# Kernel optimization log

Measured on AMD Instinct MI355X. Metric: run time of the kernel, lower is better.

Reference implementation:

```python
import jax, jax.numpy as jnp
import numpy as np

TEMP = 0.05
DIAG_PENALTY = 1e12
EPS = 1e-8  # matches torch F.cosine_similarity eps


def setup_inputs() -> dict:
    key = jax.random.key(0)
    x = jax.random.normal(key, (8192, 768), dtype=jnp.float32)
    return {"x": x}


def reference(x):
    n = x.shape[0]
    # labels: swap adjacent pairs -> i - (i%2)*2 + 1  (i.e. i XOR 1)
    idx = jnp.arange(n)
    labels = idx - (idx % 2) * 2 + 1
    # cosine similarity matrix via normalize + GEMM (same math as broadcasted
    # F.cosine_similarity: dot(x_i, x_j) / (max(||x_i||,eps) * max(||x_j||,eps)))
    norms = jnp.maximum(jnp.linalg.norm(x, axis=-1, keepdims=True), EPS)
    xn = x / norms
    sim = xn @ xn.T                                   # [N, N]
    sim = sim - jnp.eye(n, dtype=sim.dtype) * DIAG_PENALTY
    logits = sim / TEMP
    # mean cross-entropy with stable log-softmax
    logp = jax.nn.log_softmax(logits, axis=-1)
    loss = -jnp.mean(jnp.take_along_axis(logp, labels[:, None], axis=-1))
    return loss
```

## Files before the change

### kernel.cpp

```cpp
#include <hip/hip_runtime.h>
#include <hip/hip_bf16.h>

#define N 8192
#define D 768
#define TEMP_INV 20.0f
#define NTILES 2080

typedef __attribute__((ext_vector_type(4))) float f32x4;
typedef __attribute__((ext_vector_type(4))) int i32x4;
typedef __attribute__((ext_vector_type(8))) int i32x8;

#define SCALE1 0x7F7F7F7F


__global__ __launch_bounds__(256) void norm_kernel(
    const float* __restrict__ x, unsigned char* __restrict__ xn,
    float* __restrict__ rowsum) {
  int t = threadIdx.x, w = t >> 6, lane = t & 63;
  int row = blockIdx.x * 4 + w;
  const float4* xr = (const float4*)(x + (size_t)row * D);
  float4 v[3];
  v[0] = xr[lane];
  v[1] = xr[lane + 64];
  v[2] = xr[lane + 128];
  float ss = 0.0f;
#pragma unroll
  for (int i = 0; i < 3; ++i)
    ss += v[i].x * v[i].x + v[i].y * v[i].y + v[i].z * v[i].z + v[i].w * v[i].w;
#pragma unroll
  for (int m = 32; m; m >>= 1) ss += __shfl_xor(ss, m);
  float inv = 1.0f / fmaxf(sqrtf(ss), 1e-8f);
  unsigned int* xo = (unsigned int*)(xn + (size_t)row * D);
#pragma unroll
  for (int i = 0; i < 3; ++i) {
    int p = __builtin_amdgcn_cvt_pk_fp8_f32(v[i].x * inv, v[i].y * inv, 0, false);
    p = __builtin_amdgcn_cvt_pk_fp8_f32(v[i].z * inv, v[i].w * inv, p, true);
    xo[lane + 64 * i] = p;
  }
  if (t < 4) rowsum[blockIdx.x * 4 + t] = 0.0f;
}

__global__ __launch_bounds__(256, 4) void sim_kernel(
    const unsigned char* __restrict__ xn, float* __restrict__ rowsum,
    float* __restrict__ pos) {
  static const short stbase[37] = {
      0, 36, 100, 164, 228, 292, 356, 420,
      484, 520, 584, 648, 712, 776, 840,
      904, 940, 1004, 1068, 1132, 1196,
      1260, 1296, 1360, 1424, 1488,
      1552, 1588, 1652, 1716,
      1780, 1816, 1880,
      1944, 1980,
      2044, 2080};
  static const char sti[36] = {0,0,0,0,0,0,0,0, 1,1,1,1,1,1,1, 2,2,2,2,2,2,
                               3,3,3,3,3, 4,4,4,4, 5,5,5, 6,6, 7};
  static const char stj[36] = {0,1,2,3,4,5,6,7, 1,2,3,4,5,6,7, 2,3,4,5,6,7,
                               3,4,5,6,7, 4,5,6,7, 5,6,7, 6,7, 7};
  int b = blockIdx.x;
  int p = 260 * (b & 7) + (b >> 3);
  int s = 0;
  while ((int)stbase[s + 1] <= p) ++s;
  int wofs = p - stbase[s];
  int SI = sti[s], SJ = stj[s];
  int bi, bj;
  if (SI == SJ) {
    int di = 0, cum = 0;
    while (wofs >= cum + (8 - di)) { cum += 8 - di; ++di; }
    bi = SI * 8 + di;
    bj = SI * 8 + di + (wofs - cum);
  } else {
    bi = SI * 8 + (wofs >> 3);
    bj = SJ * 8 + (wofs & 7);
  }

  __shared__ i32x4 As4[128 * 8];
  __shared__ i32x4 Bs4[128 * 8];

  int t = threadIdx.x;
  int w = t >> 6, lane = t & 63;
  int q = lane >> 4, cl = lane & 15;
  int wm = w >> 1, wn = w & 1;

  f32x4 acc[4][4] = {};

  int ulog = (((t & 7) ^ ((t >> 3) & 7))) * 16;
  const unsigned char* Ab = xn + (size_t)(bi * 128 + (t >> 3)) * D + ulog;
  const unsigned char* Bb = xn + (size_t)(bj * 128 + (t >> 3)) * D + ulog;

  int u0 = (2 * q) ^ (cl & 7);
  int u1 = u0 ^ 1;

  for (int kc = 0; kc < 6; ++kc) {
    int k0 = kc * 128;
#pragma unroll
    for (int rr = 0; rr < 4; ++rr) {
      __builtin_amdgcn_global_load_lds(
          (const __attribute__((address_space(1))) unsigned int*)(Ab + (size_t)(rr * 32) * D + k0),
          (__attribute__((address_space(3))) unsigned int*)(As4 + rr * 256 + t), 16, 0, 0);
      __builtin_amdgcn_global_load_lds(
          (const __attribute__((address_space(1))) unsigned int*)(Bb + (size_t)(rr * 32) * D + k0),
          (__attribute__((address_space(3))) unsigned int*)(Bs4 + rr * 256 + t), 16, 0, 0);
    }
    __syncthreads();

    union Frag { i32x8 v8; struct { i32x4 lo, hi; } pr; };
    Frag a[4], bb[4];
#pragma unroll
    for (int m = 0; m < 4; ++m) {
      int rowb = (wm * 64 + m * 16 + cl) * 8;
      a[m].pr.lo = As4[rowb + u0];
      a[m].pr.hi = As4[rowb + u1];
    }
#pragma unroll
    for (int n = 0; n < 4; ++n) {
      int rowb = (wn * 64 + n * 16 + cl) * 8;
      bb[n].pr.lo = Bs4[rowb + u0];
      bb[n].pr.hi = Bs4[rowb + u1];
    }
#pragma unroll
    for (int m = 0; m < 4; ++m)
#pragma unroll
      for (int n = 0; n < 4; ++n)
        acc[m][n] = __builtin_amdgcn_mfma_scale_f32_16x16x128_f8f6f4(
            a[m].v8, bb[n].v8, acc[m][n], 0, 0, 0, SCALE1, 0, SCALE1);
    __syncthreads();
  }

  int gi0 = bi * 128 + wm * 64;
  int gj0 = bj * 128 + wn * 64;

  float rowp[4][4] = {};
  float colp[4] = {};

  if (bi == bj) {
#pragma unroll
    for (int m = 0; m < 4; ++m)
#pragma unroll
      for (int n = 0; n < 4; ++n)
#pragma unroll
        for (int r = 0; r < 4; ++r) {
          float sv = acc[m][n][r];
          int row = gi0 + m * 16 + q * 4 + r;
          int col = gj0 + n * 16 + cl;
          float e = __expf(TEMP_INV * sv - 20.0f);
          if (col == row) e = 0.0f;
          if (col == (row ^ 1)) pos[row] = TEMP_INV * sv;
          rowp[m][r] += e;
        }
  } else {
#pragma unroll
    for (int m = 0; m < 4; ++m)
#pragma unroll
      for (int n = 0; n < 4; ++n)
#pragma unroll
        for (int r = 0; r < 4; ++r) {
          float e = __expf(TEMP_INV * acc[m][n][r] - 20.0f);
          rowp[m][r] += e;
          colp[n] += e;
        }
  }

#pragma unroll
  for (int m = 0; m < 4; ++m)
#pragma unroll
    for (int r = 0; r < 4; ++r) {
      float v = rowp[m][r];
      v += __shfl_xor(v, 1);
      v += __shfl_xor(v, 2);
      v += __shfl_xor(v, 4);
      v += __shfl_xor(v, 8);
      if (cl == 0) atomicAdd(&rowsum[gi0 + m * 16 + q * 4 + r], v);
    }
  if (bi != bj) {
#pragma unroll
    for (int n = 0; n < 4; ++n) {
      float v = colp[n];
      v += __shfl_xor(v, 16);
      v += __shfl_xor(v, 32);
      if (q == 0) atomicAdd(&rowsum[gj0 + n * 16 + cl], v);
    }
  }
}

__global__ __launch_bounds__(1024) void loss_kernel(
    const float* __restrict__ rowsum, const float* __restrict__ pos,
    float* __restrict__ out) {
  int t = threadIdx.x;
  const float4* r4 = (const float4*)rowsum;
  const float4* p4 = (const float4*)pos;
  float acc = 0.0f;
#pragma unroll
  for (int it = 0; it < 2; ++it) {
    int i = t + it * 1024;
    float4 r = r4[i], pp = p4[i];
    acc += 80.0f + __logf(r.x) + __logf(r.y) + __logf(r.z) + __logf(r.w)
           - pp.x - pp.y - pp.z - pp.w;
  }
#pragma unroll
  for (int m = 32; m; m >>= 1) acc += __shfl_xor(acc, m);
  __shared__ float wsum[16];
  if ((t & 63) == 0) wsum[t >> 6] = acc;
  __syncthreads();
  if (t == 0) {
    float tot = 0.0f;
#pragma unroll
    for (int i = 0; i < 16; ++i) tot += wsum[i];
    out[0] = tot / (float)N;
  }
}

extern "C" void kernel_launch(void* const* d_in, const int* in_sizes, int n_in,
                              void* d_out, int out_size, void* d_ws, size_t ws_size,
                              hipStream_t stream) {
  const float* x = (const float*)d_in[0];
  float* rowsum = (float*)d_ws;
  float* pos = rowsum + N;
  unsigned char* xn = (unsigned char*)(rowsum + 2 * N + 16);

  norm_kernel<<<N / 4, 256, 0, stream>>>(x, xn, rowsum);
  sim_kernel<<<NTILES, 256, 0, stream>>>(xn, rowsum, pos);
  loss_kernel<<<1, 1024, 0, stream>>>(rowsum, pos, (float*)d_out);
}
```

Before: 125.0 us.

## Load MFMA fragments directly from global memory, dropping LDS staging and barriers

The similarity kernel no longer stages A and B tiles in shared memory through global_load_lds with barriers. Each lane now loads its FP8 MFMA fragments straight from global memory, the k-loop is fully unrolled, and the launch bound is relaxed to 2 blocks per CU so the compiler has more registers. This removes the LDS round trip and the __syncthreads stalls. In exchange, the tiles shared by the four waves are fetched redundantly from L2/global with less coalesced 32-byte accesses, and occupancy drops.

After: 193.1 us. +54.5%, slower.

```diff
diff --git a/kernel.cpp b/kernel.cpp
--- a/kernel.cpp
+++ b/kernel.cpp
@@ -40,7 +40,7 @@
   if (t < 4) rowsum[blockIdx.x * 4 + t] = 0.0f;
 }
 
-__global__ __launch_bounds__(256, 4) void sim_kernel(
+__global__ __launch_bounds__(256, 2) void sim_kernel(
     const unsigned char* __restrict__ xn, float* __restrict__ rowsum,
     float* __restrict__ pos) {
   static const short stbase[37] = {
@@ -73,9 +73,6 @@
     bj = SJ * 8 + (wofs & 7);
   }
 
-  __shared__ i32x4 As4[128 * 8];
-  __shared__ i32x4 Bs4[128 * 8];
-
   int t = threadIdx.x;
   int w = t >> 6, lane = t & 63;
   int q = lane >> 4, cl = lane & 15;
@@ -83,39 +80,25 @@
 
   f32x4 acc[4][4] = {};
 
-  int ulog = (((t & 7) ^ ((t >> 3) & 7))) * 16;
-  const unsigned char* Ab = xn + (size_t)(bi * 128 + (t >> 3)) * D + ulog;
-  const unsigned char* Bb = xn + (size_t)(bj * 128 + (t >> 3)) * D + ulog;
-
-  int u0 = (2 * q) ^ (cl & 7);
-  int u1 = u0 ^ 1;
-
+  const unsigned char* Abase = xn + (size_t)(bi * 128 + wm * 64 + cl) * D + q * 32;
+  const unsigned char* Bbase = xn + (size_t)(bj * 128 + wn * 64 + cl) * D + q * 32;
+
+  union Frag { i32x8 v8; struct { i32x4 lo, hi; } pr; };
+
+#pragma unroll
   for (int kc = 0; kc < 6; ++kc) {
-    int k0 = kc * 128;
-#pragma unroll
-    for (int rr = 0; rr < 4; ++rr) {
-      __builtin_amdgcn_global_load_lds(
-          (const __attribute__((address_space(1))) unsigned int*)(Ab + (size_t)(rr * 32) * D + k0),
-          (__attribute__((address_space(3))) unsigned int*)(As4 + rr * 256 + t), 16, 0, 0);
-      __builtin_amdgcn_global_load_lds(
-          (const __attribute__((address_space(1))) unsigned int*)(Bb + (size_t)(rr * 32) * D + k0),
-          (__attribute__((address_space(3))) unsigned int*)(Bs4 + rr * 256 + t), 16, 0, 0);
-    }
-    __syncthreads();
-
-    union Frag { i32x8 v8; struct { i32x4 lo, hi; } pr; };
     Frag a[4], bb[4];
 #pragma unroll
     for (int m = 0; m < 4; ++m) {
-      int rowb = (wm * 64 + m * 16 + cl) * 8;
-      a[m].pr.lo = As4[rowb + u0];
-      a[m].pr.hi = As4[rowb + u1];
+      const i32x4* pA = (const i32x4*)(Abase + (size_t)(m * 16) * D + kc * 128);
+      a[m].pr.lo = pA[0];
+      a[m].pr.hi = pA[1];
     }
 #pragma unroll
     for (int n = 0; n < 4; ++n) {
-      int rowb = (wn * 64 + n * 16 + cl) * 8;
-      bb[n].pr.lo = Bs4[rowb + u0];
-      bb[n].pr.hi = Bs4[rowb + u1];
+      const i32x4* pB = (const i32x4*)(Bbase + (size_t)(n * 16) * D + kc * 128);
+      bb[n].pr.lo = pB[0];
+      bb[n].pr.hi = pB[1];
     }
 #pragma unroll
     for (int m = 0; m < 4; ++m)
@@ -123,7 +106,6 @@
       for (int n = 0; n < 4; ++n)
         acc[m][n] = __builtin_amdgcn_mfma_scale_f32_16x16x128_f8f6f4(
             a[m].v8, bb[n].v8, acc[m][n], 0, 0, 0, SCALE1, 0, SCALE1);
-    __syncthreads();
   }
 
   int gi0 = bi * 128 + wm * 64;
```
